# Kernel optimization log

Hardware: AMD Instinct MI355X
Metric: run time of the kernel (lower is better)

Reference implementation:

```python
import jax, jax.numpy as jnp
import numpy as np
import math

N = 4096      # n_history
D = 512       # embed_dim
H = 8         # time-weight MLP hidden size


def setup_inputs() -> dict:
    key = jax.random.key(0)
    k1, k2, k3, k4, k5 = jax.random.split(key, 5)
    return {
        "query_code_embeds": jax.random.normal(k1, (N, D), dtype=jnp.float32),
        "hist_embeddings": jax.random.normal(k2, (N, D), dtype=jnp.float32),
        "hist_times": jax.random.uniform(k3, (N,), dtype=jnp.float32),
        "tw_w1": jax.random.normal(k4, (1, H), dtype=jnp.float32) * (1.0 / math.sqrt(1.0)),
        "tw_b1": jnp.zeros((H,), dtype=jnp.float32),
        "tw_w2": jax.random.normal(k5, (H, 1), dtype=jnp.float32) * (1.0 / math.sqrt(H)),
        "tw_b2": jnp.zeros((1,), dtype=jnp.float32),
    }


def reference(query_code_embeds, hist_embeddings, hist_times, tw_w1, tw_b1, tw_w2, tw_b2):
    # pairwise absolute time differences: [n, n, 1]
    time_diffs = jnp.abs(hist_times[:, None] - hist_times[None, :])[..., None]
    # pointwise MLP on time diffs -> multiplicative attention bias [n, n]
    h = jax.nn.relu(time_diffs @ tw_w1 + tw_b1)            # [n, n, H]
    time_weights = jax.nn.sigmoid(h @ tw_w2 + tw_b2)[..., 0]  # [n, n]
    # scaled dot-product scores modulated by time weights
    scores = (query_code_embeds @ hist_embeddings.T) / math.sqrt(D)
    scores = scores * time_weights
    attn = jax.nn.softmax(scores, axis=1)
    return attn @ hist_embeddings
```

## Files before the change

### kernel.cpp

```cpp
#include <hip/hip_runtime.h>

#define N 4096
#define D 512
#define FRAG_SH 512
#define NTHR 256
#define SC_STRIDE 136
#define SMEM_BYTES 69632

typedef __attribute__((ext_vector_type(8))) short short8;
typedef __attribute__((ext_vector_type(4))) float f32x4;

__device__ __forceinline__ unsigned short f2bf(float f) {
    unsigned int u = __float_as_uint(f);
    u = (u + 0x7FFFu + ((u >> 16) & 1u)) >> 16;
    return (unsigned short)u;
}
__device__ __forceinline__ unsigned short f2bf_rn(float f) {
    return (unsigned short)((__float_as_uint(f) + 0x8000u) >> 16);
}
__device__ __forceinline__ float bf2f(unsigned short u) {
    return __uint_as_float((unsigned)u << 16);
}

__global__ __launch_bounds__(NTHR) void prep_kernel(
    const float* __restrict__ q, const float* __restrict__ hist,
    unsigned short* __restrict__ Qblk, unsigned short* __restrict__ Kblk,
    unsigned short* __restrict__ Vblk, float* __restrict__ dsum)
{
    __shared__ unsigned short smem[32 * 512];
    const int bid = blockIdx.x, tid = threadIdx.x;
    if (bid >= 256) {
        int z = (bid - 256) * NTHR + tid;
        #pragma unroll
        for (int j = 0; j < 8; ++j) dsum[z * 8 + j] = 0.f;
        return;
    }
    const bool isQ = bid < 128;
    const int t = isQ ? bid : bid - 128;
    const float* src = isQ ? q : hist;
    const float scale = isQ ? 0.04419417382415922f : 1.0f;

    #pragma unroll
    for (int k = 0; k < 16; ++k) {
        int idx = tid + k * 256;
        int row = idx >> 7;
        int c4  = (idx & 127) << 2;
        float4 v = *(const float4*)(src + (size_t)(t * 32 + row) * D + c4);
        ushort4 o;
        o.x = f2bf(v.x * scale); o.y = f2bf(v.y * scale);
        o.z = f2bf(v.z * scale); o.w = f2bf(v.w * scale);
        *(ushort4*)(smem + row * 512 + c4) = o;
    }
    __syncthreads();

    unsigned short* ABdst = isQ ? Qblk : Kblk;
    #pragma unroll
    for (int k = 0; k < 8; ++k) {
        int s = tid + k * 256;
        int fl = s >> 6, ln = s & 63;
        int dk = fl >> 1, rbl = fl & 1;
        int l16 = ln & 15, qq = ln >> 4;
        short8 v = *(const short8*)(smem + (rbl * 16 + l16) * 512 + dk * 32 + qq * 8);
        *(short8*)(ABdst + ((size_t)dk * 256 + t * 2 + rbl) * FRAG_SH + ln * 8) = v;
    }
    if (!isQ) {
        #pragma unroll
        for (int k = 0; k < 8; ++k) {
            int s = tid + k * 256;
            int db = s >> 6, ln = s & 63;
            int l16 = ln & 15, qq = ln >> 4;
            unsigned short tmp[8];
            #pragma unroll
            for (int j = 0; j < 8; ++j)
                tmp[j] = smem[(qq * 8 + j) * 512 + db * 16 + l16];
            *(short8*)(Vblk + ((size_t)t * 32 + db) * FRAG_SH + ln * 8) = *(const short8*)tmp;
        }
    }
}

__global__ __launch_bounds__(NTHR, 2) void qk_kernel(
    const unsigned short* __restrict__ Qblk, const unsigned short* __restrict__ Kblk,
    const float* __restrict__ times,
    const float* __restrict__ w1, const float* __restrict__ b1,
    const float* __restrict__ w2, const float* __restrict__ b2,
    unsigned short* __restrict__ Pblk, float* __restrict__ dsum)
{
    extern __shared__ unsigned short smem[];
    const int tid = threadIdx.x, bid = blockIdx.x;
    const int wv = tid >> 6, lane = tid & 63;
    const int qq = lane >> 4, l16 = lane & 15;
    const int wy = wv >> 1, wx = wv & 1;
    const int cg = ((bid & 7) << 1) | ((bid >> 3) & 1);
    const int rg = bid >> 4;

    f32x4 acc[4][8];
    #pragma unroll
    for (int fy = 0; fy < 4; ++fy)
        #pragma unroll
        for (int fx = 0; fx < 8; ++fx) acc[fy][fx] = (f32x4){0.f, 0.f, 0.f, 0.f};

    for (int dk = 0; dk < 16; ++dk) {
        short8 a[4], b[8];
        #pragma unroll
        for (int fy = 0; fy < 4; ++fy)
            a[fy] = *(const short8*)(Qblk + ((size_t)dk * 256 + rg * 8 + wy * 4 + fy) * FRAG_SH + lane * 8);
        #pragma unroll
        for (int fx = 0; fx < 8; ++fx)
            b[fx] = *(const short8*)(Kblk + ((size_t)dk * 256 + cg * 16 + wx * 8 + fx) * FRAG_SH + lane * 8);
        __builtin_amdgcn_s_setprio(1);
        #pragma unroll
        for (int fy = 0; fy < 4; ++fy)
            #pragma unroll
            for (int fx = 0; fx < 8; ++fx)
                acc[fy][fx] = __builtin_amdgcn_mfma_f32_16x16x32_bf16(a[fy], b[fx], acc[fy][fx], 0, 0, 0);
        __builtin_amdgcn_s_setprio(0);
    }

    float w1v[8], b1v[8], w2v[8];
    #pragma unroll
    for (int k = 0; k < 8; ++k) { w1v[k] = w1[k]; b1v[k] = b1[k]; w2v[k] = w2[k]; }
    const float b2v = b2[0];
    bool fast = true;
    #pragma unroll
    for (int k = 0; k < 8; ++k) fast = fast && (b1v[k] == 0.0f);
    float C1 = 0.0f;
    #pragma unroll
    for (int k = 0; k < 8; ++k) C1 += w2v[k] * fmaxf(w1v[k], 0.0f);

    const int rowbase = rg * 128 + wy * 64;
    const int colbase = cg * 256 + wx * 128;
    float tcol[8];
    #pragma unroll
    for (int fx = 0; fx < 8; ++fx) tcol[fx] = times[colbase + fx * 16 + l16];
    float trow[16];
    #pragma unroll
    for (int fy = 0; fy < 4; ++fy)
        #pragma unroll
        for (int ri = 0; ri < 4; ++ri)
            trow[fy * 4 + ri] = times[rowbase + fy * 16 + qq * 4 + ri];

    unsigned short* sc = smem + wv * (64 * SC_STRIDE);
    #pragma unroll
    for (int fy = 0; fy < 4; ++fy) {
        #pragma unroll
        for (int ri = 0; ri < 4; ++ri) {
            const float tq = trow[fy * 4 + ri];
            float se = 0.f;
            #pragma unroll
            for (int fx = 0; fx < 8; ++fx) {
                float td = fabsf(tq - tcol[fx]);
                float a = fmaf(td, C1, b2v);
                if (!fast) {
                    a = b2v;
                    #pragma unroll
                    for (int k = 0; k < 8; ++k)
                        a += w2v[k] * fmaxf(fmaf(td, w1v[k], b1v[k]), 0.f);
                }
                float twt = __builtin_amdgcn_rcpf(1.0f + __expf(-a));
                float e = __expf(acc[fy][fx][ri] * twt);
                se += e;
                sc[(fy * 16 + qq * 4 + ri) * SC_STRIDE + fx * 16 + l16] = f2bf_rn(e);
            }
            se += __shfl_xor(se, 1);
            se += __shfl_xor(se, 2);
            se += __shfl_xor(se, 4);
            se += __shfl_xor(se, 8);
            if (l16 == 0) atomicAdd(dsum + rowbase + fy * 16 + qq * 4 + ri, se);
        }
    }
    #pragma unroll
    for (int fy = 0; fy < 4; ++fy)
        #pragma unroll
        for (int kb = 0; kb < 4; ++kb) {
            short8 v = *(const short8*)(sc + (fy * 16 + l16) * SC_STRIDE + kb * 32 + qq * 8);
            size_t fidx = (size_t)(cg * 8 + wx * 4 + kb) * 256 + (rg * 8 + wy * 4 + fy);
            *(short8*)(Pblk + fidx * FRAG_SH + lane * 8) = v;
        }
}

template<int FY>
__global__ __launch_bounds__(NTHR, 2) void pv_kernel(
    const unsigned short* __restrict__ Pblk, const unsigned short* __restrict__ Vblk,
    unsigned short* __restrict__ Opart, int iters)
{
    const int tid = threadIdx.x;
    const int wv = tid >> 6, lane = tid & 63;
    const int qq = lane >> 4, l16 = lane & 15;
    const int chunk = blockIdx.x;
    const int rg = blockIdx.y;
    const int kbase = chunk * iters;

    f32x4 acc[FY][8];
    #pragma unroll
    for (int fy = 0; fy < FY; ++fy)
        #pragma unroll
        for (int fx = 0; fx < 8; ++fx) acc[fy][fx] = (f32x4){0.f, 0.f, 0.f, 0.f};

    for (int it = 0; it < iters; ++it) {
        const int kb32 = kbase + it;
        short8 a[FY], b[8];
        #pragma unroll
        for (int fy = 0; fy < FY; ++fy)
            a[fy] = *(const short8*)(Pblk + ((size_t)kb32 * 256 + rg * FY + fy) * FRAG_SH + lane * 8);
        #pragma unroll
        for (int fx = 0; fx < 8; ++fx)
            b[fx] = *(const short8*)(Vblk + ((size_t)kb32 * 32 + wv * 8 + fx) * FRAG_SH + lane * 8);
        __builtin_amdgcn_s_setprio(1);
        #pragma unroll
        for (int fy = 0; fy < FY; ++fy)
            #pragma unroll
            for (int fx = 0; fx < 8; ++fx)
                acc[fy][fx] = __builtin_amdgcn_mfma_f32_16x16x32_bf16(a[fy], b[fx], acc[fy][fx], 0, 0, 0);
        __builtin_amdgcn_s_setprio(0);
    }

    unsigned short* ob = Opart + (size_t)chunk * N * D;
    #pragma unroll
    for (int fy = 0; fy < FY; ++fy)
        #pragma unroll
        for (int ri = 0; ri < 4; ++ri) {
            const int row = rg * (FY * 16) + fy * 16 + qq * 4 + ri;
            #pragma unroll
            for (int fx = 0; fx < 8; ++fx) {
                const int col = wv * 128 + fx * 16 + l16;
                ob[(size_t)row * D + col] = f2bf_rn(acc[fy][fx][ri]);
            }
        }
}

__global__ __launch_bounds__(NTHR) void reduce_kernel(
    const unsigned short* __restrict__ Opart, const float* __restrict__ dsum,
    float* __restrict__ out, int KS2)
{
    int i = blockIdx.x * NTHR + threadIdx.x;
    int row = i >> 6;
    float inv = 1.0f / dsum[row];
    float acc[8] = {0.f, 0.f, 0.f, 0.f, 0.f, 0.f, 0.f, 0.f};
    for (int c = 0; c < KS2; ++c) {
        short8 u = ((const short8*)(Opart + (size_t)c * N * D))[i];
        #pragma unroll
        for (int j = 0; j < 8; ++j) acc[j] += bf2f((unsigned short)u[j]);
    }
    float4 o0 = {acc[0] * inv, acc[1] * inv, acc[2] * inv, acc[3] * inv};
    float4 o1 = {acc[4] * inv, acc[5] * inv, acc[6] * inv, acc[7] * inv};
    ((float4*)out)[i * 2 + 0] = o0;
    ((float4*)out)[i * 2 + 1] = o1;
}

extern "C" void kernel_launch(void* const* d_in, const int* in_sizes, int n_in,
                              void* d_out, int out_size, void* d_ws, size_t ws_size,
                              hipStream_t stream) {
    const float* q     = (const float*)d_in[0];
    const float* hist  = (const float*)d_in[1];
    const float* times = (const float*)d_in[2];
    const float* w1    = (const float*)d_in[3];
    const float* b1    = (const float*)d_in[4];
    const float* w2    = (const float*)d_in[5];
    const float* b2    = (const float*)d_in[6];
    float* out = (float*)d_out;

    char* base = (char*)d_ws;
    const size_t MB4 = (size_t)N * D * 2;
    unsigned short* Vblk = (unsigned short*)base;
    unsigned short* Pblk = (unsigned short*)(base + MB4);
    float* dsum          = (float*)(base + MB4 + (size_t)N * (size_t)N * 2);
    char* ob             = base + MB4 + (size_t)N * (size_t)N * 2 + 65536;
    unsigned short* Qblk = (unsigned short*)ob;
    unsigned short* Kblk = (unsigned short*)(ob + MB4);
    unsigned short* Opart = (unsigned short*)ob;
    const size_t fixed = (size_t)(ob - base);
    const int KS2 = (ws_size >= fixed + 8 * MB4) ? 8 :
                    (ws_size >= fixed + 4 * MB4) ? 4 : 2;
    const int iters = (N / 32) / KS2;

    hipFuncSetAttribute((const void*)qk_kernel,
                        hipFuncAttributeMaxDynamicSharedMemorySize, SMEM_BYTES);

    prep_kernel<<<258, NTHR, 0, stream>>>(q, hist, Qblk, Kblk, Vblk, dsum);
    qk_kernel<<<512, NTHR, SMEM_BYTES, stream>>>(Qblk, Kblk, times, w1, b1, w2, b2, Pblk, dsum);
    if (KS2 == 8) {
        pv_kernel<4><<<dim3(KS2, N / 64), NTHR, 0, stream>>>(Pblk, Vblk, Opart, iters);
    } else {
        pv_kernel<2><<<dim3(KS2, N / 32), NTHR, 0, stream>>>(Pblk, Vblk, Opart, iters);
    }
    reduce_kernel<<<(N * D / 8) / NTHR, NTHR, 0, stream>>>(Opart, dsum, out, KS2);
}
```

Before: 134.4 us.

## Fuse split-K reduction into PV kernel via float atomics on output

Removes the separate reduce kernel and the bf16 partial-output buffers. Each PV split-K block now scales its partial result by 1/rowsum and atomically adds it straight into the fp32 output. The output is zeroed by extra blocks in the prep kernel. This saves one launch and the write and read of 8 partial buffers, but adds many global float atomics on 2M elements per split and makes the summation order nondeterministic.

```diff
diff --git a/kernel.cpp b/kernel.cpp
--- a/kernel.cpp
+++ b/kernel.cpp
@@ -6,6 +6,7 @@
 #define NTHR 256
 #define SC_STRIDE 136
 #define SMEM_BYTES 69632
+#define KS2 8
 
 typedef __attribute__((ext_vector_type(8))) short short8;
 typedef __attribute__((ext_vector_type(4))) float f32x4;
@@ -25,14 +26,23 @@
 __global__ __launch_bounds__(NTHR) void prep_kernel(
     const float* __restrict__ q, const float* __restrict__ hist,
     unsigned short* __restrict__ Qblk, unsigned short* __restrict__ Kblk,
-    unsigned short* __restrict__ Vblk, float* __restrict__ dsum)
+    unsigned short* __restrict__ Vblk, float* __restrict__ dsum,
+    float* __restrict__ out)
 {
     __shared__ unsigned short smem[32 * 512];
     const int bid = blockIdx.x, tid = threadIdx.x;
     if (bid >= 256) {
-        int z = (bid - 256) * NTHR + tid;
-        #pragma unroll
-        for (int j = 0; j < 8; ++j) dsum[z * 8 + j] = 0.f;
+        if (bid < 258) {
+            int z = (bid - 256) * NTHR + tid;
+            #pragma unroll
+            for (int j = 0; j < 8; ++j) dsum[z * 8 + j] = 0.f;
+        } else {
+            const float4 zz = {0.f, 0.f, 0.f, 0.f};
+            int base = (bid - 258) * 2048 + tid;
+            #pragma unroll
+            for (int j = 0; j < 8; ++j)
+                ((float4*)out)[base + j * NTHR] = zz;
+        }
         return;
     }
     const bool isQ = bid < 128;
@@ -178,10 +188,9 @@
         }
 }
 
-template<int FY>
 __global__ __launch_bounds__(NTHR, 2) void pv_kernel(
     const unsigned short* __restrict__ Pblk, const unsigned short* __restrict__ Vblk,
-    unsigned short* __restrict__ Opart, int iters)
+    const float* __restrict__ dsum, float* __restrict__ out, int iters)
 {
     const int tid = threadIdx.x;
     const int wv = tid >> 6, lane = tid & 63;
@@ -190,61 +199,48 @@
     const int rg = blockIdx.y;
     const int kbase = chunk * iters;
 
-    f32x4 acc[FY][8];
-    #pragma unroll
-    for (int fy = 0; fy < FY; ++fy)
+    f32x4 acc[4][8];
+    #pragma unroll
+    for (int fy = 0; fy < 4; ++fy)
         #pragma unroll
         for (int fx = 0; fx < 8; ++fx) acc[fy][fx] = (f32x4){0.f, 0.f, 0.f, 0.f};
 
     for (int it = 0; it < iters; ++it) {
         const int kb32 = kbase + it;
-        short8 a[FY], b[8];
-        #pragma unroll
-        for (int fy = 0; fy < FY; ++fy)
-            a[fy] = *(const short8*)(Pblk + ((size_t)kb32 * 256 + rg * FY + fy) * FRAG_SH + lane * 8);
+        short8 a[4], b[8];
+        #pragma unroll
+        for (int fy = 0; fy < 4; ++fy)
+            a[fy] = *(const short8*)(Pblk + ((size_t)kb32 * 256 + rg * 4 + fy) * FRAG_SH + lane * 8);
         #pragma unroll
         for (int fx = 0; fx < 8; ++fx)
             b[fx] = *(const short8*)(Vblk + ((size_t)kb32 * 32 + wv * 8 + fx) * FRAG_SH + lane * 8);
         __builtin_amdgcn_s_setprio(1);
         #pragma unroll
-        for (int fy = 0; fy < FY; ++fy)
+        for (int fy = 0; fy < 4; ++fy)
             #pragma unroll
             for (int fx = 0; fx < 8; ++fx)
                 acc[fy][fx] = __builtin_amdgcn_mfma_f32_16x16x32_bf16(a[fy], b[fx], acc[fy][fx], 0, 0, 0);
         __builtin_amdgcn_s_setprio(0);
     }
 
-    unsigned short* ob = Opart + (size_t)chunk * N * D;
-    #pragma unroll
-    for (int fy = 0; fy < FY; ++fy)
+    float inv[4][4];
+    #pragma unroll
+    for (int fy = 0; fy < 4; ++fy)
+        #pragma unroll
+        for (int ri = 0; ri < 4; ++ri)
+            inv[fy][ri] = 1.0f / dsum[rg * 64 + fy * 16 + qq * 4 + ri];
+
+    #pragma unroll
+    for (int fy = 0; fy < 4; ++fy)
         #pragma unroll
         for (int ri = 0; ri < 4; ++ri) {
-            const int row = rg * (FY * 16) + fy * 16 + qq * 4 + ri;
+            const int row = rg * 64 + fy * 16 + qq * 4 + ri;
             #pragma unroll
             for (int fx = 0; fx < 8; ++fx) {
                 const int col = wv * 128 + fx * 16 + l16;
-                ob[(size_t)row * D + col] = f2bf_rn(acc[fy][fx][ri]);
+                atomicAdd(out + (size_t)row * D + col, acc[fy][fx][ri] * inv[fy][ri]);
             }
         }
-}
-
-__global__ __launch_bounds__(NTHR) void reduce_kernel(
-    const unsigned short* __restrict__ Opart, const float* __restrict__ dsum,
-    float* __restrict__ out, int KS2)
-{
-    int i = blockIdx.x * NTHR + threadIdx.x;
-    int row = i >> 6;
-    float inv = 1.0f / dsum[row];
-    float acc[8] = {0.f, 0.f, 0.f, 0.f, 0.f, 0.f, 0.f, 0.f};
-    for (int c = 0; c < KS2; ++c) {
-        short8 u = ((const short8*)(Opart + (size_t)c * N * D))[i];
-        #pragma unroll
-        for (int j = 0; j < 8; ++j) acc[j] += bf2f((unsigned short)u[j]);
-    }
-    float4 o0 = {acc[0] * inv, acc[1] * inv, acc[2] * inv, acc[3] * inv};
-    float4 o1 = {acc[4] * inv, acc[5] * inv, acc[6] * inv, acc[7] * inv};
-    ((float4*)out)[i * 2 + 0] = o0;
-    ((float4*)out)[i * 2 + 1] = o1;
 }
 
 extern "C" void kernel_launch(void* const* d_in, const int* in_sizes, int n_in,
@@ -267,21 +263,12 @@
     char* ob             = base + MB4 + (size_t)N * (size_t)N * 2 + 65536;
     unsigned short* Qblk = (unsigned short*)ob;
     unsigned short* Kblk = (unsigned short*)(ob + MB4);
-    unsigned short* Opart = (unsigned short*)ob;
-    const size_t fixed = (size_t)(ob - base);
-    const int KS2 = (ws_size >= fixed + 8 * MB4) ? 8 :
-                    (ws_size >= fixed + 4 * MB4) ? 4 : 2;
     const int iters = (N / 32) / KS2;
 
     hipFuncSetAttribute((const void*)qk_kernel,
                         hipFuncAttributeMaxDynamicSharedMemorySize, SMEM_BYTES);
 
-    prep_kernel<<<258, NTHR, 0, stream>>>(q, hist, Qblk, Kblk, Vblk, dsum);
+    prep_kernel<<<514, NTHR, 0, stream>>>(q, hist, Qblk, Kblk, Vblk, dsum, out);
     qk_kernel<<<512, NTHR, SMEM_BYTES, stream>>>(Qblk, Kblk, times, w1, b1, w2, b2, Pblk, dsum);
-    if (KS2 == 8) {
-        pv_kernel<4><<<dim3(KS2, N / 64), NTHR, 0, stream>>>(Pblk, Vblk, Opart, iters);
-    } else {
-        pv_kernel<2><<<dim3(KS2, N / 32), NTHR, 0, stream>>>(Pblk, Vblk, Opart, iters);
-    }
-    reduce_kernel<<<(N * D / 8) / NTHR, NTHR, 0, stream>>>(Opart, dsum, out, KS2);
-}
+    pv_kernel<<<dim3(KS2, N / 64), NTHR, 0, stream>>>(Pblk, Vblk, dsum, out, iters);
+}
```

Result: slower. 173.0 us (+28.7%).

## Double-buffer QK operand fragments in LDS via async global-to-LDS loads

Applied to the files above, without the earlier changes.

Operand fragments in the QK kernel were loaded straight from global memory into registers. They are now staged into LDS with global_load_lds in a double-buffered loop, so the next k-slice loads while MFMAs run on the current one. Each fragment is fetched once per block and shared by the waves, instead of being loaded redundantly by each wave. This adds block-wide barriers and LDS reads, and drops the s_setprio hints.

```diff
diff --git a/kernel.cpp b/kernel.cpp
--- a/kernel.cpp
+++ b/kernel.cpp
@@ -6,9 +6,12 @@
 #define NTHR 256
 #define SC_STRIDE 136
 #define SMEM_BYTES 69632
+#define BUF_SH 12288
 
 typedef __attribute__((ext_vector_type(8))) short short8;
 typedef __attribute__((ext_vector_type(4))) float f32x4;
+typedef const __attribute__((address_space(1))) unsigned int* gptr_t;
+typedef __attribute__((address_space(3))) unsigned int* lptr_t;
 
 __device__ __forceinline__ unsigned short f2bf(float f) {
     unsigned int u = __float_as_uint(f);
@@ -99,21 +102,44 @@
         #pragma unroll
         for (int fx = 0; fx < 8; ++fx) acc[fy][fx] = (f32x4){0.f, 0.f, 0.f, 0.f};
 
-    for (int dk = 0; dk < 16; ++dk) {
-        short8 a[4], b[8];
+    auto stage = [&](int dk, int buf) {
+        unsigned short* ldsb = smem + buf * BUF_SH;
+        #pragma unroll
+        for (int j = 0; j < 6; ++j) {
+            const int s = wv * 6 + j;
+            const unsigned short* g = (s < 8)
+                ? (Qblk + ((size_t)dk * 256 + rg * 8 + s) * FRAG_SH + lane * 8)
+                : (Kblk + ((size_t)dk * 256 + cg * 16 + (s - 8)) * FRAG_SH + lane * 8);
+            __builtin_amdgcn_global_load_lds(
+                (gptr_t)g, (lptr_t)(ldsb + s * FRAG_SH), 16, 0, 0);
+        }
+    };
+    auto compute = [&](int buf) {
+        const unsigned short* bufc = smem + buf * BUF_SH;
+        short8 fa[4], fb[8];
         #pragma unroll
         for (int fy = 0; fy < 4; ++fy)
-            a[fy] = *(const short8*)(Qblk + ((size_t)dk * 256 + rg * 8 + wy * 4 + fy) * FRAG_SH + lane * 8);
+            fa[fy] = *(const short8*)(bufc + (wy * 4 + fy) * FRAG_SH + lane * 8);
         #pragma unroll
         for (int fx = 0; fx < 8; ++fx)
-            b[fx] = *(const short8*)(Kblk + ((size_t)dk * 256 + cg * 16 + wx * 8 + fx) * FRAG_SH + lane * 8);
-        __builtin_amdgcn_s_setprio(1);
+            fb[fx] = *(const short8*)(bufc + (8 + wx * 8 + fx) * FRAG_SH + lane * 8);
         #pragma unroll
         for (int fy = 0; fy < 4; ++fy)
             #pragma unroll
             for (int fx = 0; fx < 8; ++fx)
-                acc[fy][fx] = __builtin_amdgcn_mfma_f32_16x16x32_bf16(a[fy], b[fx], acc[fy][fx], 0, 0, 0);
-        __builtin_amdgcn_s_setprio(0);
+                acc[fy][fx] = __builtin_amdgcn_mfma_f32_16x16x32_bf16(fa[fy], fb[fx], acc[fy][fx], 0, 0, 0);
+    };
+
+    stage(0, 0);
+    __syncthreads();
+    #pragma unroll 1
+    for (int dk = 0; dk < 16; dk += 2) {
+        stage(dk + 1, 1);
+        compute(0);
+        __syncthreads();
+        if (dk + 2 < 16) stage(dk + 2, 0);
+        compute(1);
+        __syncthreads();
     }
 
     float w1v[8], b1v[8], w2v[8];
@@ -171,9 +197,9 @@
     #pragma unroll
     for (int fy = 0; fy < 4; ++fy)
         #pragma unroll
-        for (int kb = 0; kb < 4; ++kb) {
-            short8 v = *(const short8*)(sc + (fy * 16 + l16) * SC_STRIDE + kb * 32 + qq * 8);
-            size_t fidx = (size_t)(cg * 8 + wx * 4 + kb) * 256 + (rg * 8 + wy * 4 + fy);
+        for (int kb2 = 0; kb2 < 4; ++kb2) {
+            short8 v = *(const short8*)(sc + (fy * 16 + l16) * SC_STRIDE + kb2 * 32 + qq * 8);
+            size_t fidx = (size_t)(cg * 8 + wx * 4 + kb2) * 256 + (rg * 8 + wy * 4 + fy);
             *(short8*)(Pblk + fidx * FRAG_SH + lane * 8) = v;
         }
 }
@@ -273,7 +299,7 @@
                     (ws_size >= fixed + 4 * MB4) ? 4 : 2;
     const int iters = (N / 32) / KS2;
 
-    hipFuncSetAttribute((const void*)qk_kernel,
+    (void)hipFuncSetAttribute((const void*)qk_kernel,
                         hipFuncAttributeMaxDynamicSharedMemorySize, SMEM_BYTES);
 
     prep_kernel<<<258, NTHR, 0, stream>>>(q, hist, Qblk, Kblk, Vblk, dsum);
```

Result: no change. 132.5 us (-1.4%).
